# Kernel optimization log

Hardware: AMD Instinct MI355X
Metric: run time of the kernel (lower is better)

## Reference

```python
import jax, jax.numpy as jnp
import numpy as np

N_NODES = 20000
N_EDGES = 320000
HID = 128
EPS = 1e-8

def _linear_params(key, fan_in, fan_out):
    k1, k2 = jax.random.split(key)
    bound = 1.0 / np.sqrt(fan_in)
    W = jax.random.uniform(k1, (fan_in, fan_out), jnp.float32, -bound, bound)
    b = jax.random.uniform(k2, (fan_out,), jnp.float32, -bound, bound)
    return W, b

def setup_inputs() -> dict:
    key = jax.random.key(0)
    ks = jax.random.split(key, 12)
    h = jax.random.normal(ks[0], (N_NODES, HID), jnp.float32)
    coord = jax.random.normal(ks[1], (N_NODES, 3), jnp.float32)
    row = jax.random.randint(ks[2], (N_EDGES,), 0, N_NODES)
    # guarantee no self-loops (norm^(-1-alpha) would blow up)
    off = jax.random.randint(ks[3], (N_EDGES,), 1, N_NODES)
    col = (row + off) % N_NODES
    edges = jnp.stack([row, col], axis=0).astype(jnp.int64)
    W_ce1, b_ce1 = _linear_params(ks[4], 2 * HID, HID)
    W_ce2, b_ce2 = _linear_params(ks[5], HID, HID)
    W_pe1, b_pe1 = _linear_params(ks[6], 18, HID)
    W_pe2, b_pe2 = _linear_params(ks[7], HID, HID)
    W_s1, b_s1 = _linear_params(ks[8], HID, HID)
    W_s2, b_s2 = _linear_params(ks[9], HID, HID)
    W_att, b_att = _linear_params(ks[10], HID, 1)
    return dict(h=h, coord=coord, edges=edges,
                W_ce1=W_ce1, b_ce1=b_ce1, W_ce2=W_ce2, b_ce2=b_ce2,
                W_pe1=W_pe1, b_pe1=b_pe1, W_pe2=W_pe2, b_pe2=b_pe2,
                W_s1=W_s1, b_s1=b_s1, W_s2=W_s2, b_s2=b_s2,
                W_att=W_att, b_att=b_att)

def _mlp(x, W1, b1, W2, b2):
    # Linear -> SiLU -> (Dropout, eval: identity) -> Linear
    return jax.nn.silu(x @ W1 + b1) @ W2 + b2

def _forward(h, coord, row, col,
             W_ce1, b_ce1, W_ce2, b_ce2, W_pe1, b_pe1, W_pe2, b_pe2,
             W_s1, b_s1, W_s2, b_s2, W_att, b_att):
    coord_diff = coord[row] - coord[col]                       # [E,3]
    init_radial = jnp.sum(coord_diff ** 2, axis=1, keepdims=True)  # [E,1]
    # radial: 15 Gaussian-like scales, exp(-0.5/2.25^s * r^2)
    scales = jnp.asarray([-0.5 / 2.25 ** s for s in range(15)], jnp.float32)
    radial = jnp.exp(init_radial * scales[None, :])            # [E,15]
    dnorm = jnp.linalg.norm(coord_diff, axis=-1, keepdims=True)  # [E,1]
    coord_diff_n = coord_diff / (dnorm + EPS)                  # normalized [E,3]
    # coord2nforce: per-order segment means of |d|^(-1-alpha) * d, normalized
    n = coord.shape[0]
    cnt = jax.ops.segment_sum(jnp.ones((row.shape[0],), jnp.float32), row,
                              num_segments=n)
    denom = jnp.maximum(cnt, 1.0)[:, None]                     # [N,1]
    nvec_list = []
    for alpha in (2, 3, 4):
        ordered = dnorm ** (-1.0 - alpha) * coord_diff         # [E,3]
        nforce = jax.ops.segment_sum(ordered, row, num_segments=n) / denom
        nforce = nforce / (jnp.linalg.norm(nforce, axis=-1, keepdims=True) + EPS)
        nvec_list.append(nforce)
    nvecs = jnp.stack(nvec_list, axis=1)                       # [N,3,3]
    nprod = jnp.sum(nvecs[row] * nvecs[col], axis=-1)          # [E,3]
    chem_in = jnp.concatenate([h[row], h[col]], axis=1)        # [E,2H]
    pos_in = jnp.concatenate([nprod, radial], axis=1)          # [E,18]
    chem = _mlp(chem_in, W_ce1, b_ce1, W_ce2, b_ce2)           # [E,H]
    pos = _mlp(pos_in, W_pe1, b_pe1, W_pe2, b_pe2)             # [E,H]
    out = _mlp(chem, W_s1, b_s1, W_s2, b_s2) * pos             # [E,H]
    att_val = jax.nn.sigmoid(out @ W_att + b_att)              # [E,1]
    out = out * att_val
    return out, chem, pos, coord_diff_n

def reference(h, coord, edges,
              W_ce1, b_ce1, W_ce2, b_ce2, W_pe1, b_pe1, W_pe2, b_pe2,
              W_s1, b_s1, W_s2, b_s2, W_att, b_att):
    row, col = edges[0], edges[1]
    return _forward(h, coord, row, col,
                    W_ce1, b_ce1, W_ce2, b_ce2, W_pe1, b_pe1, W_pe2, b_pe2,
                    W_s1, b_s1, W_s2, b_s2, W_att, b_att)
```

## Files before the change

### kernel.cpp

```cpp
#include <hip/hip_runtime.h>

#define E_EDGES 320000
#define NN 20000
#define HID 128
#define TS 136

typedef __attribute__((ext_vector_type(8))) short short8;
typedef __attribute__((ext_vector_type(4))) float f32x4;
typedef __attribute__((ext_vector_type(8))) unsigned short us8;
typedef __attribute__((ext_vector_type(4))) unsigned uint4v;

__device__ __forceinline__ unsigned short f2b(float f) {
  unsigned u = __builtin_bit_cast(unsigned, f);
  u += 0x7fffu + ((u >> 16) & 1u);
  return (unsigned short)(u >> 16);
}
__device__ __forceinline__ unsigned cvt_pk_bf16(float lo, float hi) {
  unsigned r;
  asm("v_cvt_pk_bf16_f32 %0, %1, %2" : "=v"(r) : "v"(lo), "v"(hi));
  return r;
}
#define LOG2E 1.44269504f
__device__ __forceinline__ float fast_sigmoid(float x) {
  return __builtin_amdgcn_rcpf(1.0f + __builtin_amdgcn_exp2f(-x * LOG2E));
}
__device__ __forceinline__ float silu_f(float x) { return x * fast_sigmoid(x); }

__global__ void prepack_k(const float* __restrict__ Wce1, const float* __restrict__ Wce2,
                          const float* __restrict__ Ws1,  const float* __restrict__ Ws2,
                          const float* __restrict__ Wpe2, const float* __restrict__ Wpe1,
                          unsigned short* __restrict__ dst, float* __restrict__ nf) {
  int b = blockIdx.x;
  if (b >= 400) {
    int j = (b - 400) * 256 + threadIdx.x;
    if (j < NN * 9 / 4)
      reinterpret_cast<float4*>(nf)[j] = float4{0.0f, 0.0f, 0.0f, 0.0f};
    return;
  }
  int i = b * 256 + threadIdx.x;
  const float* W; int Ksrc, base;
  if (i < 32768)      { W = Wce1; Ksrc = 256; base = 0; }
  else if (i < 49152) { W = Wce2; Ksrc = 128; base = 32768; }
  else if (i < 65536) { W = Ws1;  Ksrc = 128; base = 49152; }
  else if (i < 81920) { W = Ws2;  Ksrc = 128; base = 65536; }
  else if (i < 98304) { W = Wpe2; Ksrc = 128; base = 81920; }
  else                { W = Wpe1; Ksrc = 18;  base = 98304; }
  int j = i - base;
  int r = j & 7, lane = (j >> 3) & 63, ntg = (j >> 9) & 7, kt = j >> 12;
  int sk = kt * 32 + ((lane >> 4) << 3) + r;
  int sn = (ntg << 4) + (lane & 15);
  float v = (sk < Ksrc) ? W[sk * HID + sn] : 0.0f;
  dst[i] = f2b(v);
}

__global__ void edge_geom_k(const int* __restrict__ erow, const int* __restrict__ ecol,
                            const float* __restrict__ coord,
                            float* __restrict__ nf,
                            float* __restrict__ cdn, unsigned short* __restrict__ rad16) {
  int i = blockIdx.x * 256 + threadIdx.x;
  if (i >= E_EDGES) return;
  int r = erow[i], c = ecol[i];
  float dx = coord[r*3+0] - coord[c*3+0];
  float dy = coord[r*3+1] - coord[c*3+1];
  float dz = coord[r*3+2] - coord[c*3+2];
  float r2 = dx*dx + dy*dy + dz*dz;
  float dn = sqrtf(r2);
  float invn = __builtin_amdgcn_rcpf(dn + 1e-8f);
  cdn[i*3+0] = dx*invn; cdn[i*3+1] = dy*invn; cdn[i*3+2] = dz*invn;

  unsigned short rv[16];
  float t = 1.0f;
  #pragma unroll
  for (int s = 0; s < 15; s++) {
    rv[s] = f2b(__builtin_amdgcn_exp2f(r2 * (-0.5f * LOG2E) / t));
    t *= 2.25f;
  }
  rv[15] = 0;
  us8 lo, hi;
  #pragma unroll
  for (int k = 0; k < 8; k++) { lo[k] = rv[k]; hi[k] = rv[8+k]; }
  *reinterpret_cast<us8*>(rad16 + (size_t)i*16)     = lo;
  *reinterpret_cast<us8*>(rad16 + (size_t)i*16 + 8) = hi;

  float inv = __builtin_amdgcn_rcpf(dn);
  float w3 = inv*inv*inv, w4 = w3*inv, w5 = w4*inv;
  float* p = nf + r*9;
  unsafeAtomicAdd(p+0, w3*dx); unsafeAtomicAdd(p+1, w3*dy); unsafeAtomicAdd(p+2, w3*dz);
  unsafeAtomicAdd(p+3, w4*dx); unsafeAtomicAdd(p+4, w4*dy); unsafeAtomicAdd(p+5, w4*dz);
  unsafeAtomicAdd(p+6, w5*dx); unsafeAtomicAdd(p+7, w5*dy); unsafeAtomicAdd(p+8, w5*dz);
}

__global__ __launch_bounds__(256) void node_k(
    const float* __restrict__ h, const unsigned short* __restrict__ wp,
    const float* __restrict__ b1, const float* __restrict__ nf,
    float* __restrict__ nvecs,
    unsigned short* __restrict__ Htb, unsigned short* __restrict__ Hbb) {
  int b = blockIdx.x;
  if (b >= 625) {
    int n = (b - 625) * 256 + threadIdx.x;
    if (n >= NN) return;
    #pragma unroll
    for (int a = 0; a < 3; a++) {
      float x = nf[n*9+a*3+0], y = nf[n*9+a*3+1], z = nf[n*9+a*3+2];
      float nm = sqrtf(x*x + y*y + z*z);
      float s = __builtin_amdgcn_rcpf(nm + 1e-8f);
      nvecs[n*9+a*3+0] = x*s; nvecs[n*9+a*3+1] = y*s; nvecs[n*9+a*3+2] = z*s;
    }
    return;
  }
  const int tid = threadIdx.x, lane = tid & 63, wv = tid >> 6;
  const int cl = lane & 15, kg = lane >> 4;
  const int w = b * 4 + wv;
  const int half = w & 1;
  const int n0 = (w >> 1) * 16;

  f32x4 acc[8];
  #pragma unroll
  for (int nt = 0; nt < 8; nt++) {
    float bb = half ? 0.0f : b1[nt*16 + cl];
    acc[nt] = f32x4{bb, bb, bb, bb};
  }
  #pragma unroll
  for (int k4 = 0; k4 < 4; k4++) {
    int kt = half*4 + k4;
    const float* hp = h + (size_t)(n0 + cl) * HID + k4*32 + kg*8;
    float4 v0 = *reinterpret_cast<const float4*>(hp);
    float4 v1 = *reinterpret_cast<const float4*>(hp + 4);
    unsigned p0 = cvt_pk_bf16(v0.x, v0.y), p1 = cvt_pk_bf16(v0.z, v0.w);
    unsigned p2 = cvt_pk_bf16(v1.x, v1.y), p3 = cvt_pk_bf16(v1.z, v1.w);
    short8 af = __builtin_bit_cast(short8, uint4v{p0, p1, p2, p3});
    #pragma unroll
    for (int nt = 0; nt < 8; nt++) {
      short8 bf = *reinterpret_cast<const short8*>(wp + ((kt*8 + nt)*64 + lane)*8);
      acc[nt] = __builtin_amdgcn_mfma_f32_16x16x32_bf16(af, bf, acc[nt], 0, 0, 0);
    }
  }
  unsigned short* dst = half ? Hbb : Htb;
  #pragma unroll
  for (int nt = 0; nt < 8; nt++) {
    unsigned q0 = cvt_pk_bf16(acc[nt][0], acc[nt][1]);
    unsigned q1 = cvt_pk_bf16(acc[nt][2], acc[nt][3]);
    dst[(size_t)(n0 + kg*4 + 0) * HID + nt*16 + cl] = (unsigned short)(q0 & 0xffff);
    dst[(size_t)(n0 + kg*4 + 1) * HID + nt*16 + cl] = (unsigned short)(q0 >> 16);
    dst[(size_t)(n0 + kg*4 + 2) * HID + nt*16 + cl] = (unsigned short)(q1 & 0xffff);
    dst[(size_t)(n0 + kg*4 + 3) * HID + nt*16 + cl] = (unsigned short)(q1 >> 16);
  }
}

__global__ __launch_bounds__(256, 4) void edge_mlp_k(
    const int* __restrict__ erow, const int* __restrict__ ecol,
    const unsigned short* __restrict__ Htb, const unsigned short* __restrict__ Hbb,
    const unsigned short* __restrict__ rad16, const float* __restrict__ nvecs,
    const unsigned short* __restrict__ wp,
    const float* __restrict__ b2,  const float* __restrict__ bs1,
    const float* __restrict__ bs2, const float* __restrict__ bp1,
    const float* __restrict__ bp2,
    const float* __restrict__ watt, const float* __restrict__ batt,
    float* __restrict__ out0, float* __restrict__ chem_o, float* __restrict__ pos_o) {
  __shared__ unsigned short sT[4][16 * TS];
  const int tid = threadIdx.x, lane = tid & 63, wv = tid >> 6;
  const int cl = lane & 15, kg = lane >> 4;
  const int e0 = (blockIdx.x * 4 + wv) * 16;
  unsigned short* T = sT[wv];

  const int er_ = erow[e0 + cl];
  const int ec_ = ecol[e0 + cl];

  us8 r0 = *reinterpret_cast<const us8*>(rad16 + (size_t)(e0 + cl)*16);
  us8 r1 = *reinterpret_cast<const us8*>(rad16 + (size_t)(e0 + cl)*16 + 8);
  float np[3];
  if (kg == 0) {
    #pragma unroll
    for (int a = 0; a < 3; a++)
      np[a] = nvecs[er_*9+a*3+0]*nvecs[ec_*9+a*3+0]
            + nvecs[er_*9+a*3+1]*nvecs[ec_*9+a*3+1]
            + nvecs[er_*9+a*3+2]*nvecs[ec_*9+a*3+2];
  }

  f32x4 acc[8];
  #pragma unroll
  for (int nt = 0; nt < 8; nt++) {
    float bb = b2[nt*16 + cl];
    acc[nt] = f32x4{bb, bb, bb, bb};
  }
  #pragma unroll
  for (int kt = 0; kt < 4; kt++) {
    uint4v ta = *reinterpret_cast<const uint4v*>(Htb + (size_t)er_ * HID + kt*32 + kg*8);
    uint4v tb = *reinterpret_cast<const uint4v*>(Hbb + (size_t)ec_ * HID + kt*32 + kg*8);
    unsigned pw[4];
    #pragma unroll
    for (int p = 0; p < 4; p++) {
      float alo = __builtin_bit_cast(float, ta[p] << 16);
      float ahi = __builtin_bit_cast(float, ta[p] & 0xffff0000u);
      float blo = __builtin_bit_cast(float, tb[p] << 16);
      float bhi = __builtin_bit_cast(float, tb[p] & 0xffff0000u);
      pw[p] = cvt_pk_bf16(silu_f(alo + blo), silu_f(ahi + bhi));
    }
    short8 af = __builtin_bit_cast(short8, uint4v{pw[0], pw[1], pw[2], pw[3]});
    #pragma unroll
    for (int nt = 0; nt < 8; nt++) {
      short8 bf = *reinterpret_cast<const short8*>(wp + 32768 + ((kt*8 + nt)*64 + lane)*8);
      acc[nt] = __builtin_amdgcn_mfma_f32_16x16x32_bf16(af, bf, acc[nt], 0, 0, 0);
    }
  }
  #pragma unroll
  for (int nt = 0; nt < 8; nt++) {
    #pragma unroll
    for (int g = 0; g < 4; g++)
      chem_o[(size_t)(e0 + kg*4 + g) * HID + nt*16 + cl] = acc[nt][g];
    unsigned q0 = cvt_pk_bf16(acc[nt][0], acc[nt][1]);
    unsigned q1 = cvt_pk_bf16(acc[nt][2], acc[nt][3]);
    T[(kg*4 + 0)*TS + nt*16 + cl] = (unsigned short)(q0 & 0xffff);
    T[(kg*4 + 1)*TS + nt*16 + cl] = (unsigned short)(q0 >> 16);
    T[(kg*4 + 2)*TS + nt*16 + cl] = (unsigned short)(q1 & 0xffff);
    T[(kg*4 + 3)*TS + nt*16 + cl] = (unsigned short)(q1 >> 16);
  }

  #pragma unroll
  for (int nt = 0; nt < 8; nt++) {
    float bb = bs1[nt*16 + cl];
    acc[nt] = f32x4{bb, bb, bb, bb};
  }
  #pragma unroll
  for (int kt = 0; kt < 4; kt++) {
    short8 af = *reinterpret_cast<const short8*>(T + cl*TS + kt*32 + kg*8);
    #pragma unroll
    for (int nt = 0; nt < 8; nt++) {
      short8 bf = *reinterpret_cast<const short8*>(wp + 49152 + ((kt*8 + nt)*64 + lane)*8);
      acc[nt] = __builtin_amdgcn_mfma_f32_16x16x32_bf16(af, bf, acc[nt], 0, 0, 0);
    }
  }
  #pragma unroll
  for (int nt = 0; nt < 8; nt++) {
    unsigned q0 = cvt_pk_bf16(silu_f(acc[nt][0]), silu_f(acc[nt][1]));
    unsigned q1 = cvt_pk_bf16(silu_f(acc[nt][2]), silu_f(acc[nt][3]));
    T[(kg*4 + 0)*TS + nt*16 + cl] = (unsigned short)(q0 & 0xffff);
    T[(kg*4 + 1)*TS + nt*16 + cl] = (unsigned short)(q0 >> 16);
    T[(kg*4 + 2)*TS + nt*16 + cl] = (unsigned short)(q1 & 0xffff);
    T[(kg*4 + 3)*TS + nt*16 + cl] = (unsigned short)(q1 >> 16);
  }

  f32x4 accS[8];
  #pragma unroll
  for (int nt = 0; nt < 8; nt++) {
    float bb = bs2[nt*16 + cl];
    accS[nt] = f32x4{bb, bb, bb, bb};
  }
  #pragma unroll
  for (int kt = 0; kt < 4; kt++) {
    short8 af = *reinterpret_cast<const short8*>(T + cl*TS + kt*32 + kg*8);
    #pragma unroll
    for (int nt = 0; nt < 8; nt++) {
      short8 bf = *reinterpret_cast<const short8*>(wp + 65536 + ((kt*8 + nt)*64 + lane)*8);
      accS[nt] = __builtin_amdgcn_mfma_f32_16x16x32_bf16(af, bf, accS[nt], 0, 0, 0);
    }
  }

  #pragma unroll
  for (int nt = 0; nt < 8; nt++) {
    float bb = bp1[nt*16 + cl];
    acc[nt] = f32x4{bb, bb, bb, bb};
  }
  {
    short8 af;
    if (kg == 0) {
      af[0]=(short)f2b(np[0]); af[1]=(short)f2b(np[1]); af[2]=(short)f2b(np[2]);
      af[3]=(short)r0[0]; af[4]=(short)r0[1]; af[5]=(short)r0[2];
      af[6]=(short)r0[3]; af[7]=(short)r0[4];
    } else if (kg == 1) {
      af[0]=(short)r0[5]; af[1]=(short)r0[6]; af[2]=(short)r0[7];
      af[3]=(short)r1[0]; af[4]=(short)r1[1]; af[5]=(short)r1[2];
      af[6]=(short)r1[3]; af[7]=(short)r1[4];
    } else if (kg == 2) {
      af[0]=(short)r1[5]; af[1]=(short)r1[6];
      af[2]=0; af[3]=0; af[4]=0; af[5]=0; af[6]=0; af[7]=0;
    } else {
      af[0]=0; af[1]=0; af[2]=0; af[3]=0; af[4]=0; af[5]=0; af[6]=0; af[7]=0;
    }
    #pragma unroll
    for (int nt = 0; nt < 8; nt++) {
      short8 bf = *reinterpret_cast<const short8*>(wp + 98304 + (nt*64 + lane)*8);
      acc[nt] = __builtin_amdgcn_mfma_f32_16x16x32_bf16(af, bf, acc[nt], 0, 0, 0);
    }
  }
  #pragma unroll
  for (int nt = 0; nt < 8; nt++) {
    unsigned q0 = cvt_pk_bf16(silu_f(acc[nt][0]), silu_f(acc[nt][1]));
    unsigned q1 = cvt_pk_bf16(silu_f(acc[nt][2]), silu_f(acc[nt][3]));
    T[(kg*4 + 0)*TS + nt*16 + cl] = (unsigned short)(q0 & 0xffff);
    T[(kg*4 + 1)*TS + nt*16 + cl] = (unsigned short)(q0 >> 16);
    T[(kg*4 + 2)*TS + nt*16 + cl] = (unsigned short)(q1 & 0xffff);
    T[(kg*4 + 3)*TS + nt*16 + cl] = (unsigned short)(q1 >> 16);
  }

  float ps[4] = {0,0,0,0};
  #pragma unroll
  for (int half = 0; half < 2; half++) {
    f32x4 ph[4];
    #pragma unroll
    for (int n4 = 0; n4 < 4; n4++) {
      float bb = bp2[(half*4 + n4)*16 + cl];
      ph[n4] = f32x4{bb, bb, bb, bb};
    }
    #pragma unroll
    for (int kt = 0; kt < 4; kt++) {
      short8 af = *reinterpret_cast<const short8*>(T + cl*TS + kt*32 + kg*8);
      #pragma unroll
      for (int n4 = 0; n4 < 4; n4++) {
        short8 bf = *reinterpret_cast<const short8*>(wp + 81920 + ((kt*8 + half*4 + n4)*64 + lane)*8);
        ph[n4] = __builtin_amdgcn_mfma_f32_16x16x32_bf16(af, bf, ph[n4], 0, 0, 0);
      }
    }
    #pragma unroll
    for (int n4 = 0; n4 < 4; n4++) {
      int nt = half*4 + n4;
      float wa = watt[nt*16 + cl];
      #pragma unroll
      for (int g = 0; g < 4; g++) {
        float p = ph[n4][g];
        pos_o[(size_t)(e0 + kg*4 + g) * HID + nt*16 + cl] = p;
        float o = accS[nt][g] * p;
        accS[nt][g] = o;
        ps[g] += o * wa;
      }
    }
  }

  float ba = batt[0];
  #pragma unroll
  for (int g = 0; g < 4; g++) {
    float s = ps[g];
    s += __shfl_xor(s, 1);
    s += __shfl_xor(s, 2);
    s += __shfl_xor(s, 4);
    s += __shfl_xor(s, 8);
    float av = fast_sigmoid(s + ba);
    #pragma unroll
    for (int nt = 0; nt < 8; nt++)
      out0[(size_t)(e0 + kg*4 + g) * HID + nt*16 + cl] = accS[nt][g] * av;
  }
}

extern "C" void kernel_launch(void* const* d_in, const int* in_sizes, int n_in,
                              void* d_out, int out_size, void* d_ws, size_t ws_size,
                              hipStream_t stream) {
  (void)in_sizes; (void)n_in; (void)out_size; (void)ws_size;
  const float* h     = (const float*)d_in[0];
  const float* coord = (const float*)d_in[1];
  const int*   edges = (const int*)d_in[2];
  const float* W_ce1 = (const float*)d_in[3];  const float* b_ce1 = (const float*)d_in[4];
  const float* W_ce2 = (const float*)d_in[5];  const float* b_ce2 = (const float*)d_in[6];
  const float* W_pe1 = (const float*)d_in[7];  const float* b_pe1 = (const float*)d_in[8];
  const float* W_pe2 = (const float*)d_in[9];  const float* b_pe2 = (const float*)d_in[10];
  const float* W_s1  = (const float*)d_in[11]; const float* b_s1  = (const float*)d_in[12];
  const float* W_s2  = (const float*)d_in[13]; const float* b_s2  = (const float*)d_in[14];
  const float* W_att = (const float*)d_in[15]; const float* b_att = (const float*)d_in[16];

  float* out  = (float*)d_out;
  float* chem = out  + (size_t)E_EDGES * HID;
  float* pos  = chem + (size_t)E_EDGES * HID;
  float* cdn  = pos  + (size_t)E_EDGES * HID;

  char* ws = (char*)d_ws;
  float* nf    = (float*)(ws);
  float* nvecs = (float*)(ws + 720000);
  unsigned short* Htb   = (unsigned short*)(ws + 1440000);
  unsigned short* Hbb   = (unsigned short*)(ws + 6560000);
  unsigned short* wpack = (unsigned short*)(ws + 11680000);
  unsigned short* rad16 = (unsigned short*)(ws + 11884800);

  prepack_k<<<576, 256, 0, stream>>>(W_ce1, W_ce2, W_s1, W_s2, W_pe2, W_pe1, wpack, nf);
  edge_geom_k<<<E_EDGES / 256, 256, 0, stream>>>(edges, edges + E_EDGES, coord,
                                                 nf, cdn, rad16);
  node_k<<<704, 256, 0, stream>>>(h, wpack, b_ce1, nf, nvecs, Htb, Hbb);
  edge_mlp_k<<<E_EDGES / 64, 256, 0, stream>>>(edges, edges + E_EDGES, Htb, Hbb,
                                               rad16, nvecs, wpack,
                                               b_ce2, b_s1, b_s2, b_pe1, b_pe2,
                                               W_att, b_att, out, chem, pos);
}
```

Before: 384.4 us.

## Fuse edge geometry into node GEMM kernel, normalize node vectors on the fly

Merges the edge-geometry kernel and the node projection kernel into one launch, with block ranges split between the two roles. The separate node-vector normalization pass is dropped: the node force accumulators are padded to a 12-float stride and normalized inside the edge MLP using float4 loads. Large output writes (chem, pos, out, coord_diff_n) now use nontemporal stores to avoid polluting cache. This saves one launch and one pass over node data, at the cost of redundant per-edge normalization work and a less clean separation between the two roles in the fused kernel.

Measured after the change: 384.0 us. About the same (-0.1%).

```diff
diff --git a/kernel.cpp b/kernel.cpp
--- a/kernel.cpp
+++ b/kernel.cpp
@@ -33,7 +33,7 @@
   int b = blockIdx.x;
   if (b >= 400) {
     int j = (b - 400) * 256 + threadIdx.x;
-    if (j < NN * 9 / 4)
+    if (j < NN * 12 / 4)
       reinterpret_cast<float4*>(nf)[j] = float4{0.0f, 0.0f, 0.0f, 0.0f};
     return;
   }
@@ -53,64 +53,52 @@
   dst[i] = f2b(v);
 }
 
-__global__ void edge_geom_k(const int* __restrict__ erow, const int* __restrict__ ecol,
-                            const float* __restrict__ coord,
-                            float* __restrict__ nf,
-                            float* __restrict__ cdn, unsigned short* __restrict__ rad16) {
-  int i = blockIdx.x * 256 + threadIdx.x;
-  if (i >= E_EDGES) return;
-  int r = erow[i], c = ecol[i];
-  float dx = coord[r*3+0] - coord[c*3+0];
-  float dy = coord[r*3+1] - coord[c*3+1];
-  float dz = coord[r*3+2] - coord[c*3+2];
-  float r2 = dx*dx + dy*dy + dz*dz;
-  float dn = sqrtf(r2);
-  float invn = __builtin_amdgcn_rcpf(dn + 1e-8f);
-  cdn[i*3+0] = dx*invn; cdn[i*3+1] = dy*invn; cdn[i*3+2] = dz*invn;
-
-  unsigned short rv[16];
-  float t = 1.0f;
-  #pragma unroll
-  for (int s = 0; s < 15; s++) {
-    rv[s] = f2b(__builtin_amdgcn_exp2f(r2 * (-0.5f * LOG2E) / t));
-    t *= 2.25f;
-  }
-  rv[15] = 0;
-  us8 lo, hi;
-  #pragma unroll
-  for (int k = 0; k < 8; k++) { lo[k] = rv[k]; hi[k] = rv[8+k]; }
-  *reinterpret_cast<us8*>(rad16 + (size_t)i*16)     = lo;
-  *reinterpret_cast<us8*>(rad16 + (size_t)i*16 + 8) = hi;
-
-  float inv = __builtin_amdgcn_rcpf(dn);
-  float w3 = inv*inv*inv, w4 = w3*inv, w5 = w4*inv;
-  float* p = nf + r*9;
-  unsafeAtomicAdd(p+0, w3*dx); unsafeAtomicAdd(p+1, w3*dy); unsafeAtomicAdd(p+2, w3*dz);
-  unsafeAtomicAdd(p+3, w4*dx); unsafeAtomicAdd(p+4, w4*dy); unsafeAtomicAdd(p+5, w4*dz);
-  unsafeAtomicAdd(p+6, w5*dx); unsafeAtomicAdd(p+7, w5*dy); unsafeAtomicAdd(p+8, w5*dz);
-}
-
-__global__ __launch_bounds__(256) void node_k(
-    const float* __restrict__ h, const unsigned short* __restrict__ wp,
-    const float* __restrict__ b1, const float* __restrict__ nf,
-    float* __restrict__ nvecs,
+__global__ __launch_bounds__(256) void geomnode_k(
+    const int* __restrict__ erow, const int* __restrict__ ecol,
+    const float* __restrict__ coord, const float* __restrict__ h,
+    const unsigned short* __restrict__ wp, const float* __restrict__ b1,
+    float* __restrict__ nf, unsigned short* __restrict__ rad16,
+    float* __restrict__ cdn,
     unsigned short* __restrict__ Htb, unsigned short* __restrict__ Hbb) {
   int b = blockIdx.x;
-  if (b >= 625) {
-    int n = (b - 625) * 256 + threadIdx.x;
-    if (n >= NN) return;
-    #pragma unroll
-    for (int a = 0; a < 3; a++) {
-      float x = nf[n*9+a*3+0], y = nf[n*9+a*3+1], z = nf[n*9+a*3+2];
-      float nm = sqrtf(x*x + y*y + z*z);
-      float s = __builtin_amdgcn_rcpf(nm + 1e-8f);
-      nvecs[n*9+a*3+0] = x*s; nvecs[n*9+a*3+1] = y*s; nvecs[n*9+a*3+2] = z*s;
-    }
+  if (b < 1250) {
+    int i = b * 256 + threadIdx.x;
+    int r = erow[i], c = ecol[i];
+    float dx = coord[r*3+0] - coord[c*3+0];
+    float dy = coord[r*3+1] - coord[c*3+1];
+    float dz = coord[r*3+2] - coord[c*3+2];
+    float r2 = dx*dx + dy*dy + dz*dz;
+    float dn = sqrtf(r2);
+    float invn = __builtin_amdgcn_rcpf(dn + 1e-8f);
+    __builtin_nontemporal_store(dx*invn, &cdn[i*3+0]);
+    __builtin_nontemporal_store(dy*invn, &cdn[i*3+1]);
+    __builtin_nontemporal_store(dz*invn, &cdn[i*3+2]);
+
+    unsigned short rv[16];
+    float t = 1.0f;
+    #pragma unroll
+    for (int s = 0; s < 15; s++) {
+      rv[s] = f2b(__builtin_amdgcn_exp2f(r2 * (-0.5f * LOG2E) / t));
+      t *= 2.25f;
+    }
+    rv[15] = 0;
+    us8 lo, hi;
+    #pragma unroll
+    for (int k = 0; k < 8; k++) { lo[k] = rv[k]; hi[k] = rv[8+k]; }
+    *reinterpret_cast<us8*>(rad16 + (size_t)i*16)     = lo;
+    *reinterpret_cast<us8*>(rad16 + (size_t)i*16 + 8) = hi;
+
+    float inv = __builtin_amdgcn_rcpf(dn);
+    float w3 = inv*inv*inv, w4 = w3*inv, w5 = w4*inv;
+    float* p = nf + r*12;
+    unsafeAtomicAdd(p+0, w3*dx); unsafeAtomicAdd(p+1, w3*dy); unsafeAtomicAdd(p+2, w3*dz);
+    unsafeAtomicAdd(p+3, w4*dx); unsafeAtomicAdd(p+4, w4*dy); unsafeAtomicAdd(p+5, w4*dz);
+    unsafeAtomicAdd(p+6, w5*dx); unsafeAtomicAdd(p+7, w5*dy); unsafeAtomicAdd(p+8, w5*dz);
     return;
   }
   const int tid = threadIdx.x, lane = tid & 63, wv = tid >> 6;
   const int cl = lane & 15, kg = lane >> 4;
-  const int w = b * 4 + wv;
+  const int w = (b - 1250) * 4 + wv;
   const int half = w & 1;
   const int n0 = (w >> 1) * 16;
 
@@ -150,7 +138,7 @@
 __global__ __launch_bounds__(256, 4) void edge_mlp_k(
     const int* __restrict__ erow, const int* __restrict__ ecol,
     const unsigned short* __restrict__ Htb, const unsigned short* __restrict__ Hbb,
-    const unsigned short* __restrict__ rad16, const float* __restrict__ nvecs,
+    const unsigned short* __restrict__ rad16, const float* __restrict__ nf,
     const unsigned short* __restrict__ wp,
     const float* __restrict__ b2,  const float* __restrict__ bs1,
     const float* __restrict__ bs2, const float* __restrict__ bp1,
@@ -170,11 +158,31 @@
   us8 r1 = *reinterpret_cast<const us8*>(rad16 + (size_t)(e0 + cl)*16 + 8);
   float np[3];
   if (kg == 0) {
-    #pragma unroll
-    for (int a = 0; a < 3; a++)
-      np[a] = nvecs[er_*9+a*3+0]*nvecs[ec_*9+a*3+0]
-            + nvecs[er_*9+a*3+1]*nvecs[ec_*9+a*3+1]
-            + nvecs[er_*9+a*3+2]*nvecs[ec_*9+a*3+2];
+    const float4* ap = reinterpret_cast<const float4*>(nf + er_*12);
+    const float4* bp = reinterpret_cast<const float4*>(nf + ec_*12);
+    float4 A0 = ap[0], A1 = ap[1], A2 = ap[2];
+    float4 B0 = bp[0], B1 = bp[1], B2 = bp[2];
+    {
+      float d  = A0.x*B0.x + A0.y*B0.y + A0.z*B0.z;
+      float na = A0.x*A0.x + A0.y*A0.y + A0.z*A0.z;
+      float nb = B0.x*B0.x + B0.y*B0.y + B0.z*B0.z;
+      np[0] = d * __builtin_amdgcn_rcpf(sqrtf(na) + 1e-8f)
+                * __builtin_amdgcn_rcpf(sqrtf(nb) + 1e-8f);
+    }
+    {
+      float d  = A0.w*B0.w + A1.x*B1.x + A1.y*B1.y;
+      float na = A0.w*A0.w + A1.x*A1.x + A1.y*A1.y;
+      float nb = B0.w*B0.w + B1.x*B1.x + B1.y*B1.y;
+      np[1] = d * __builtin_amdgcn_rcpf(sqrtf(na) + 1e-8f)
+                * __builtin_amdgcn_rcpf(sqrtf(nb) + 1e-8f);
+    }
+    {
+      float d  = A1.z*B1.z + A1.w*B1.w + A2.x*B2.x;
+      float na = A1.z*A1.z + A1.w*A1.w + A2.x*A2.x;
+      float nb = B1.z*B1.z + B1.w*B1.w + B2.x*B2.x;
+      np[2] = d * __builtin_amdgcn_rcpf(sqrtf(na) + 1e-8f)
+                * __builtin_amdgcn_rcpf(sqrtf(nb) + 1e-8f);
+    }
   }
 
   f32x4 acc[8];
@@ -207,7 +215,8 @@
   for (int nt = 0; nt < 8; nt++) {
     #pragma unroll
     for (int g = 0; g < 4; g++)
-      chem_o[(size_t)(e0 + kg*4 + g) * HID + nt*16 + cl] = acc[nt][g];
+      __builtin_nontemporal_store(acc[nt][g],
+          &chem_o[(size_t)(e0 + kg*4 + g) * HID + nt*16 + cl]);
     unsigned q0 = cvt_pk_bf16(acc[nt][0], acc[nt][1]);
     unsigned q1 = cvt_pk_bf16(acc[nt][2], acc[nt][3]);
     T[(kg*4 + 0)*TS + nt*16 + cl] = (unsigned short)(q0 & 0xffff);
@@ -318,7 +327,8 @@
       #pragma unroll
       for (int g = 0; g < 4; g++) {
         float p = ph[n4][g];
-        pos_o[(size_t)(e0 + kg*4 + g) * HID + nt*16 + cl] = p;
+        __builtin_nontemporal_store(p,
+            &pos_o[(size_t)(e0 + kg*4 + g) * HID + nt*16 + cl]);
         float o = accS[nt][g] * p;
         accS[nt][g] = o;
         ps[g] += o * wa;
@@ -337,7 +347,8 @@
     float av = fast_sigmoid(s + ba);
     #pragma unroll
     for (int nt = 0; nt < 8; nt++)
-      out0[(size_t)(e0 + kg*4 + g) * HID + nt*16 + cl] = accS[nt][g] * av;
+      __builtin_nontemporal_store(accS[nt][g] * av,
+          &out0[(size_t)(e0 + kg*4 + g) * HID + nt*16 + cl]);
   }
 }
 
@@ -362,19 +373,17 @@
   float* cdn  = pos  + (size_t)E_EDGES * HID;
 
   char* ws = (char*)d_ws;
-  float* nf    = (float*)(ws);
-  float* nvecs = (float*)(ws + 720000);
-  unsigned short* Htb   = (unsigned short*)(ws + 1440000);
-  unsigned short* Hbb   = (unsigned short*)(ws + 6560000);
-  unsigned short* wpack = (unsigned short*)(ws + 11680000);
-  unsigned short* rad16 = (unsigned short*)(ws + 11884800);
-
-  prepack_k<<<576, 256, 0, stream>>>(W_ce1, W_ce2, W_s1, W_s2, W_pe2, W_pe1, wpack, nf);
-  edge_geom_k<<<E_EDGES / 256, 256, 0, stream>>>(edges, edges + E_EDGES, coord,
-                                                 nf, cdn, rad16);
-  node_k<<<704, 256, 0, stream>>>(h, wpack, b_ce1, nf, nvecs, Htb, Hbb);
+  float* nf             = (float*)(ws);
+  unsigned short* Htb   = (unsigned short*)(ws + 960000);
+  unsigned short* Hbb   = (unsigned short*)(ws + 6080000);
+  unsigned short* wpack = (unsigned short*)(ws + 11200000);
+  unsigned short* rad16 = (unsigned short*)(ws + 11404800);
+
+  prepack_k<<<635, 256, 0, stream>>>(W_ce1, W_ce2, W_s1, W_s2, W_pe2, W_pe1, wpack, nf);
+  geomnode_k<<<1875, 256, 0, stream>>>(edges, edges + E_EDGES, coord, h, wpack, b_ce1,
+                                       nf, rad16, cdn, Htb, Hbb);
   edge_mlp_k<<<E_EDGES / 64, 256, 0, stream>>>(edges, edges + E_EDGES, Htb, Hbb,
-                                               rad16, nvecs, wpack,
+                                               rad16, nf, wpack,
                                                b_ce2, b_s1, b_s2, b_pe1, b_pe2,
                                                W_att, b_att, out, chem, pos);
 }
```
